# Performance work log

Measured on AMD Instinct MI355X. Metric: run time of the kernel, lower is better.

## Reference

```python
import jax, jax.numpy as jnp
import numpy as np

N, E = 50000, 800000
NODE_IN, EDGE_IN = 32, 16
EMB, GEMB = 128, 128
H, C, L, B = 4, 32, 2, 8   # heads, per-head dim, layers, graphs
GAT_IN = NODE_IN + EMB      # skip_conn=True
NEG_SLOPE = 0.2
EPS = 1e-5


def layernorm(x, g, b):
    m = jnp.mean(x, -1, keepdims=True)
    v = jnp.mean((x - m) ** 2, -1, keepdims=True)
    return (x - m) / jnp.sqrt(v + EPS) * g + b


def setup_inputs() -> dict:
    key = jax.random.key(0)
    ks = jax.random.split(key, 24)
    s = 0.05
    return {
        "x": jax.random.normal(ks[0], (N, NODE_IN), jnp.float32),
        "edge_attr": jax.random.normal(ks[1], (E, EDGE_IN), jnp.float32),
        "W_in": jax.random.normal(ks[2], (NODE_IN, EMB), jnp.float32) * s,
        "b_in": jnp.zeros((EMB,), jnp.float32),
        "W_src": jax.random.normal(ks[3], (L, GAT_IN, H * C), jnp.float32) * s,
        "W_edge": jax.random.normal(ks[4], (L, EDGE_IN, H * C), jnp.float32) * s,
        "att_src": jax.random.normal(ks[5], (L, H, C), jnp.float32) * s,
        "att_dst": jax.random.normal(ks[6], (L, H, C), jnp.float32) * s,
        "att_edge": jax.random.normal(ks[7], (L, H, C), jnp.float32) * s,
        "gat_bias": jnp.zeros((L, H * C), jnp.float32),
        "ln_gamma": jnp.ones((L, EMB), jnp.float32),
        "ln_beta": jnp.zeros((L, EMB), jnp.float32),
        "W_out": jax.random.normal(ks[8], (EMB, EMB), jnp.float32) * s,
        "b_out": jnp.zeros((EMB,), jnp.float32),
        "ln_out_gamma": jnp.ones((EMB,), jnp.float32),
        "ln_out_beta": jnp.zeros((EMB,), jnp.float32),
        "W_g": jax.random.normal(ks[9], (EMB, GEMB), jnp.float32) * s,
        "b_g": jnp.zeros((GEMB,), jnp.float32),
        "g_gamma": jnp.ones((GEMB,), jnp.float32),
        "g_beta": jnp.zeros((GEMB,), jnp.float32),
        "edge_index": jax.random.randint(ks[10], (2, E), 0, N, jnp.int32),
        "batch": jnp.sort(jax.random.randint(ks[11], (N,), 0, B, jnp.int32)),
    }


def reference(x, edge_attr, W_in, b_in, W_src, W_edge, att_src, att_dst, att_edge,
              gat_bias, ln_gamma, ln_beta, W_out, b_out, ln_out_gamma, ln_out_beta,
              W_g, b_g, g_gamma, g_beta, edge_index, batch):
    # PyG GATConv adds self-loops with edge_attr fill_value='mean'
    loop = jnp.arange(N, dtype=edge_index.dtype)
    src = jnp.concatenate([edge_index[0], loop])   # [E2]
    dst = jnp.concatenate([edge_index[1], loop])   # [E2]
    ea = jnp.concatenate([edge_attr, jnp.broadcast_to(edge_attr.mean(0), (N, EDGE_IN))], 0)

    h = jax.nn.relu(x @ W_in + b_in)  # [N, EMB]
    for l in range(L):
        inp = jnp.concatenate([x, h], -1)                   # skip connection [N, GAT_IN]
        xs = (inp @ W_src[l]).reshape(N, H, C)              # projected nodes
        a_s = jnp.einsum('nhc,hc->nh', xs, att_src[l])
        a_d = jnp.einsum('nhc,hc->nh', xs, att_dst[l])
        ee = (ea @ W_edge[l]).reshape(-1, H, C)             # [E2, H, C]
        a_e = jnp.einsum('ehc,hc->eh', ee, att_edge[l])
        alpha = jax.nn.leaky_relu(a_s[src] + a_d[dst] + a_e, NEG_SLOPE)  # [E2, H]
        # segment softmax over incoming edges of each destination node
        amax = jax.ops.segment_max(alpha, dst, num_segments=N)
        ex = jnp.exp(alpha - amax[dst])
        denom = jax.ops.segment_sum(ex, dst, num_segments=N)
        w = ex / (denom[dst] + 1e-16)
        msg = xs[src] * w[:, :, None]                        # [E2, H, C]
        out = jax.ops.segment_sum(msg, dst, num_segments=N).reshape(N, H * C) + gat_bias[l]
        h = jax.nn.elu(layernorm(out, ln_gamma[l], ln_beta[l]))

    g = layernorm(jax.nn.relu(h @ W_g + b_g), g_gamma, g_beta)
    gsum = jax.ops.segment_sum(g, batch, num_segments=B)
    cnt = jax.ops.segment_sum(jnp.ones((N, 1), g.dtype), batch, num_segments=B)
    graph_embeddings = gsum / jnp.maximum(cnt, 1.0)

    node_embeddings = layernorm(jax.nn.relu(h @ W_out + b_out), ln_out_gamma, ln_out_beta)
    return node_embeddings, graph_embeddings
```

## Files before the change

kernel.cpp:

```cpp
#include <hip/hip_runtime.h>

#define N_NODES 50000
#define N_EDGES 800000
#define E2      850000
#define NODE_IN 32
#define EDGE_IN 16
#define EMB     128
#define GAT_IN  160
#define NLAYER  2
#define NGRAPH  8
#define NBLK    196
#define NB32    1563
#define NB64    782

#define GWT_SRC0 0
#define GWT_SRC1 20480
#define GWT_OUT  40960
#define GWT_G    57344
#define GWT_TOT  73728

typedef short bf16x8 __attribute__((ext_vector_type(8)));
typedef float f32x4 __attribute__((ext_vector_type(4)));

__device__ __forceinline__ unsigned int f2bf(float f) {
    unsigned int u = __float_as_uint(f);
    return (u + 0x7FFFu + ((u >> 16) & 1u)) >> 16;
}
__device__ __forceinline__ float bf2f(unsigned int h) {
    return __uint_as_float(h << 16);
}
__device__ __forceinline__ unsigned int pack2bf(float a, float b) {
    return f2bf(a) | (f2bf(b) << 16);
}

__global__ void zero_kernel(float* __restrict__ p, int n) {
    int i = blockIdx.x * blockDim.x + threadIdx.x;
    int stride = gridDim.x * blockDim.x;
    for (; i < n; i += stride) p[i] = 0.f;
}

__global__ __launch_bounds__(256) void mean_kernel(const float* __restrict__ ea,
                                                   float* __restrict__ meta) {
    __shared__ float sm[16];
    int t = threadIdx.x;
    if (t < 16) sm[t] = 0.f;
    __syncthreads();
    int gid = blockIdx.x * 256 + t;
    int q = gid & 3;
    const float4* ea4 = (const float4*)ea;
    float4 s = make_float4(0.f, 0.f, 0.f, 0.f);
    for (int j = gid; j < N_EDGES * 4; j += 2048 * 256) {
        float4 v = ea4[j];
        s.x += v.x; s.y += v.y; s.z += v.z; s.w += v.w;
    }
    atomicAdd(&sm[q * 4 + 0], s.x);
    atomicAdd(&sm[q * 4 + 1], s.y);
    atomicAdd(&sm[q * 4 + 2], s.z);
    atomicAdd(&sm[q * 4 + 3], s.w);
    __syncthreads();
    if (t < 16) atomicAdd(&meta[t], sm[t]);
}

__global__ void prep_kernel(const float* __restrict__ W_edge,
                            const float* __restrict__ att_edge,
                            float* __restrict__ meta) {
    int t = threadIdx.x;
    if (t < EDGE_IN) meta[t] = meta[t] * (1.0f / (float)N_EDGES);
    __syncthreads();
    {
        int l = t >> 6, k = (t >> 2) & 15, h = t & 3;
        const float* w = W_edge + ((size_t)l * EDGE_IN + k) * EMB + h * 32;
        const float* a = att_edge + (size_t)l * EMB + h * 32;
        float acc = 0.f;
#pragma unroll
        for (int c = 0; c < 32; c++) acc += w[c] * a[c];
        meta[16 + (l * 16 + k) * 4 + h] = acc;
    }
    __syncthreads();
    if (t < 8) {
        int l = t >> 2, h = t & 3;
        float acc = 0.f;
#pragma unroll
        for (int k = 0; k < EDGE_IN; k++) acc += meta[k] * meta[16 + (l * 16 + k) * 4 + h];
        meta[144 + t] = acc;
    }
}

__global__ __launch_bounds__(256) void prep_wt_kernel(const float* __restrict__ Wsrc,
                                                      const float* __restrict__ Wout,
                                                      const float* __restrict__ Wg,
                                                      unsigned short* __restrict__ gwt) {
    int g = blockIdx.x * 256 + threadIdx.x;
    const float* Wm;
    int base, gg;
    if (g < 5120) {
        int l = g / 2560;
        gg = g - l * 2560;
        Wm = Wsrc + (size_t)l * GAT_IN * EMB;
        base = l * 20480;
    } else if (g < 7168) {
        gg = g - 5120;
        Wm = Wout;
        base = GWT_OUT;
    } else {
        gg = g - 7168;
        Wm = Wg;
        base = GWT_G;
    }
    int lane = gg & 63, tmp = gg >> 6;
    int nt = tmp & 7, kc = tmp >> 3;
    int quad = lane >> 4, l16 = lane & 15;
    int col = nt * 16 + l16, k0 = kc * 32 + quad * 8;
    unsigned int u[4];
#pragma unroll
    for (int j = 0; j < 4; j++)
        u[j] = pack2bf(Wm[(size_t)(k0 + 2 * j) * EMB + col], Wm[(size_t)(k0 + 2 * j + 1) * EMB + col]);
    *(uint4*)(gwt + base + (size_t)gg * 8) = make_uint4(u[0], u[1], u[2], u[3]);
}

__global__ __launch_bounds__(256) void count_rank_kernel(const int* __restrict__ edge_index,
                                                         int* __restrict__ cnt4,
                                                         int* __restrict__ rank) {
    int e = blockIdx.x * 256 + threadIdx.x;
    if (e >= E2) return;
    int dst = (e < N_EDGES) ? edge_index[N_EDGES + e] : (e - N_EDGES);
    int shard = blockIdx.x & 3;
    rank[e] = atomicAdd(&cnt4[shard * N_NODES + dst], 1);
}

__global__ __launch_bounds__(256) void scan1_kernel(const int* __restrict__ cnt4,
                                                    int* __restrict__ bsum) {
    __shared__ int sm[256];
    int t = threadIdx.x;
    int i = blockIdx.x * 256 + t;
    int tot = 0;
    if (i < N_NODES) {
#pragma unroll
        for (int s = 0; s < 4; s++) tot += cnt4[s * N_NODES + i];
    }
    sm[t] = tot;
    __syncthreads();
#pragma unroll
    for (int d = 128; d >= 1; d >>= 1) {
        if (t < d) sm[t] += sm[t + d];
        __syncthreads();
    }
    if (t == 0) bsum[blockIdx.x] = sm[0];
}

__global__ __launch_bounds__(256) void scan2_kernel(const int* __restrict__ bsum,
                                                    int* __restrict__ bbase) {
    __shared__ int sm[256];
    int t = threadIdx.x;
    int v = (t < NBLK) ? bsum[t] : 0;
    sm[t] = v;
    __syncthreads();
#pragma unroll
    for (int d = 1; d < 256; d <<= 1) {
        int u = (t >= d) ? sm[t - d] : 0;
        __syncthreads();
        sm[t] += u;
        __syncthreads();
    }
    if (t < NBLK) bbase[t] = sm[t] - v;
}

__global__ __launch_bounds__(256) void scan3_kernel(const int* __restrict__ bbase,
                                                    const int* __restrict__ cnt4,
                                                    int* __restrict__ off,
                                                    int* __restrict__ shard_base) {
    __shared__ int sm[256];
    int t = threadIdx.x;
    int i = blockIdx.x * 256 + t;
    int c[4] = {0, 0, 0, 0};
    int tot = 0;
    if (i < N_NODES) {
#pragma unroll
        for (int s = 0; s < 4; s++) {
            c[s] = cnt4[s * N_NODES + i];
            tot += c[s];
        }
    }
    sm[t] = tot;
    __syncthreads();
#pragma unroll
    for (int d = 1; d < 256; d <<= 1) {
        int u = (t >= d) ? sm[t - d] : 0;
        __syncthreads();
        sm[t] += u;
        __syncthreads();
    }
    if (i < N_NODES) {
        int base = bbase[blockIdx.x] + sm[t] - tot;
        off[i] = base;
        int4 sb;
        sb.x = base;            base += c[0];
        sb.y = base;            base += c[1];
        sb.z = base;            base += c[2];
        sb.w = base;
        *(int4*)(shard_base + i * 4) = sb;
        if (i == N_NODES - 1) off[N_NODES] = E2;
    }
}

__global__ __launch_bounds__(256) void fill_ae_kernel(const int* __restrict__ edge_index,
                                                      const float* __restrict__ edge_attr,
                                                      const float* __restrict__ meta,
                                                      const int* __restrict__ rank,
                                                      const int* __restrict__ shard_base,
                                                      int* __restrict__ csr_src,
                                                      float* __restrict__ csr_ae0,
                                                      float* __restrict__ csr_ae1) {
    __shared__ float Ml[128];
    __shared__ float loop_ae[8];
    int t = threadIdx.x;
    if (t < 128) Ml[t] = meta[16 + t];
    if (t < 8) loop_ae[t] = meta[144 + t];
    __syncthreads();
    int e = blockIdx.x * 256 + t;
    if (e >= E2) return;
    int src, dst;
    float ae[2][4];
    if (e < N_EDGES) {
        src = edge_index[e];
        dst = edge_index[N_EDGES + e];
        const float4* r4 = (const float4*)(edge_attr + (size_t)e * EDGE_IN);
#pragma unroll
        for (int l = 0; l < 2; l++)
#pragma unroll
            for (int h = 0; h < 4; h++) ae[l][h] = 0.f;
#pragma unroll
        for (int q = 0; q < 4; q++) {
            float4 v = r4[q];
#pragma unroll
            for (int l = 0; l < 2; l++) {
                const float* M = Ml + l * 64;
#pragma unroll
                for (int h = 0; h < 4; h++) {
                    ae[l][h] += v.x * M[(4 * q + 0) * 4 + h] + v.y * M[(4 * q + 1) * 4 + h] +
                                v.z * M[(4 * q + 2) * 4 + h] + v.w * M[(4 * q + 3) * 4 + h];
                }
            }
        }
    } else {
        src = dst = e - N_EDGES;
#pragma unroll
        for (int l = 0; l < 2; l++)
#pragma unroll
            for (int h = 0; h < 4; h++) ae[l][h] = loop_ae[l * 4 + h];
    }
    int shard = (e >> 8) & 3;
    int pos = shard_base[dst * 4 + shard] + rank[e];
    csr_src[pos] = src;
    *(float4*)(csr_ae0 + (size_t)pos * 4) = make_float4(ae[0][0], ae[0][1], ae[0][2], ae[0][3]);
    *(float4*)(csr_ae1 + (size_t)pos * 4) = make_float4(ae[1][0], ae[1][1], ae[1][2], ae[1][3]);
}

__global__ __launch_bounds__(256) void input_proj_kernel(const float* __restrict__ x,
                                                         const float* __restrict__ W,
                                                         const float* __restrict__ b,
                                                         unsigned int* __restrict__ h_bf,
                                                         unsigned int* __restrict__ x_bf) {
    __shared__ float inp[32][NODE_IN];
    int t = threadIdx.x;
    int n0 = blockIdx.x * 32;
    for (int i = t; i < 32 * NODE_IN; i += 256) {
        int r = i >> 5, c = i & 31;
        int n = min(n0 + r, N_NODES - 1);
        inp[r][c] = x[(size_t)n * NODE_IN + c];
    }
    __syncthreads();
    for (int i = t; i < 32 * 16; i += 256) {
        int r = i >> 4, c = i & 15;
        int n = n0 + r;
        if (n < N_NODES) x_bf[(size_t)n * 16 + c] = pack2bf(inp[r][2 * c], inp[r][2 * c + 1]);
    }
    int wave = t >> 6, lane = t & 63;
    int c0 = lane * 2, c1 = c0 + 1;
    const float2* W2 = (const float2*)W;
    float acc[8][2];
#pragma unroll
    for (int j = 0; j < 8; j++) { acc[j][0] = b[c0]; acc[j][1] = b[c1]; }
#pragma unroll 2
    for (int k4 = 0; k4 < NODE_IN / 4; k4++) {
        float4 v[8];
#pragma unroll
        for (int j = 0; j < 8; j++) v[j] = *(const float4*)&inp[wave * 8 + j][k4 * 4];
#pragma unroll
        for (int kk = 0; kk < 4; kk++) {
            float2 w = W2[(k4 * 4 + kk) * 64 + lane];
#pragma unroll
            for (int j = 0; j < 8; j++) {
                float vv = (&v[j].x)[kk];
                acc[j][0] += vv * w.x;
                acc[j][1] += vv * w.y;
            }
        }
    }
#pragma unroll
    for (int j = 0; j < 8; j++) {
        int n = n0 + wave * 8 + j;
        if (n < N_NODES)
            h_bf[(size_t)n * 64 + lane] = pack2bf(fmaxf(acc[j][0], 0.f), fmaxf(acc[j][1], 0.f));
    }
}

template <int K, int MODE>
__global__ __launch_bounds__(256) void dense_mfma_kernel(
    const unsigned int* __restrict__ xbf, const unsigned int* __restrict__ hbf,
    const unsigned short* __restrict__ gwt, const float* __restrict__ bias,
    const float* __restrict__ v1, const float* __restrict__ v2,
    const int* __restrict__ batch,
    unsigned int* __restrict__ xs_out, float* __restrict__ a_s, float* __restrict__ a_d,
    float* __restrict__ out_nodes, float* __restrict__ gsum, float* __restrict__ gcnt) {
    constexpr int CLS = 132;
    __shared__ __align__(16) float cl[64 * CLS];
    __shared__ float red[(MODE != 0) ? 64 : 1][8];
    __shared__ float locw[(MODE == 2) ? 4 : 1][2][EMB];
    __shared__ int bids[(MODE == 2) ? 64 : 1];

    int t = threadIdx.x;
    int n0 = blockIdx.x * 64;
    if (MODE == 2 && t < 64) bids[t] = batch[min(n0 + t, N_NODES - 1)];

    int wave = t >> 6, lane = t & 63;
    int quad = lane >> 4, l16 = lane & 15;
    int arow = min(n0 + wave * 16 + l16, N_NODES - 1);
    const bf16x8* B = (const bf16x8*)gwt;
    f32x4 acc[8];
#pragma unroll
    for (int i = 0; i < 8; i++) acc[i] = (f32x4){0.f, 0.f, 0.f, 0.f};
#pragma unroll
    for (int kc = 0; kc < K / 32; kc++) {
        bf16x8 af;
        if (MODE == 0 && kc == 0) {
            af = *(const bf16x8*)(xbf + (size_t)arow * 16 + quad * 4);
        } else {
            int hk = ((MODE == 0) ? (kc - 1) : kc) * 16;
            af = *(const bf16x8*)(hbf + (size_t)arow * 64 + hk + quad * 4);
        }
#pragma unroll
        for (int nt = 0; nt < 8; nt++) {
            bf16x8 bfv = B[(kc * 8 + nt) * 64 + lane];
            acc[nt] = __builtin_amdgcn_mfma_f32_16x16x32_bf16(af, bfv, acc[nt], 0, 0, 0);
        }
    }
#pragma unroll
    for (int nt = 0; nt < 8; nt++) {
#pragma unroll
        for (int i = 0; i < 4; i++) {
            int r = wave * 16 + quad * 4 + i;
            cl[r * CLS + nt * 16 + l16] = acc[nt][i];
        }
    }
    __syncthreads();

    int p = t & 3, r = t >> 2;
    int n = n0 + r;
    const float4* c4 = (const float4*)(cl + r * CLS + p * 32);

    if (MODE == 0) {
        const float4* s4 = (const float4*)(v1 + p * 32);
        const float4* d4 = (const float4*)(v2 + p * 32);
        if (n < N_NODES) {
            float s_ = 0.f, d_ = 0.f;
#pragma unroll
            for (int i = 0; i < 8; i++) {
                float4 cv = c4[i], sv = s4[i], dv = d4[i];
                s_ += cv.x * sv.x + cv.y * sv.y + cv.z * sv.z + cv.w * sv.w;
                d_ += cv.x * dv.x + cv.y * dv.y + cv.z * dv.z + cv.w * dv.w;
                uint2 pk = make_uint2(pack2bf(cv.x, cv.y), pack2bf(cv.z, cv.w));
                *(uint2*)(xs_out + (size_t)n * 64 + p * 16 + 2 * i) = pk;
            }
            a_s[(size_t)n * 4 + p] = s_;
            a_d[(size_t)n * 4 + p] = d_;
        }
    } else {
        const float4* b4 = (const float4*)(bias + p * 32);
        float vals[32];
        float s_ = 0.f, q_ = 0.f;
#pragma unroll
        for (int i = 0; i < 8; i++) {
            float4 cv = c4[i], bv = b4[i];
            float w0 = fmaxf(cv.x + bv.x, 0.f), w1 = fmaxf(cv.y + bv.y, 0.f);
            float w2 = fmaxf(cv.z + bv.z, 0.f), w3 = fmaxf(cv.w + bv.w, 0.f);
            vals[4 * i] = w0; vals[4 * i + 1] = w1; vals[4 * i + 2] = w2; vals[4 * i + 3] = w3;
            s_ += w0 + w1 + w2 + w3;
            q_ += w0 * w0 + w1 * w1 + w2 * w2 + w3 * w3;
        }
        red[r][p] = s_;
        red[r][4 + p] = q_;
        __syncthreads();
        float sm = red[r][0] + red[r][1] + red[r][2] + red[r][3];
        float sq = red[r][4] + red[r][5] + red[r][6] + red[r][7];
        float mean = sm * (1.f / EMB);
        float var = sq * (1.f / EMB) - mean * mean;
        float rstd = rsqrtf(var + 1e-5f);
        const float4* g4 = (const float4*)(v1 + p * 32);
        const float4* be4 = (const float4*)(v2 + p * 32);
#pragma unroll
        for (int i = 0; i < 8; i++) {
            float4 gv = g4[i], bv = be4[i];
            vals[4 * i]     = (vals[4 * i]     - mean) * rstd * gv.x + bv.x;
            vals[4 * i + 1] = (vals[4 * i + 1] - mean) * rstd * gv.y + bv.y;
            vals[4 * i + 2] = (vals[4 * i + 2] - mean) * rstd * gv.z + bv.z;
            vals[4 * i + 3] = (vals[4 * i + 3] - mean) * rstd * gv.w + bv.w;
        }
        if (MODE == 1) {
            if (n < N_NODES) {
                float* op = out_nodes + (size_t)n * EMB + p * 32;
#pragma unroll
                for (int i = 0; i < 8; i++)
                    *(float4*)(op + 4 * i) = make_float4(vals[4 * i], vals[4 * i + 1],
                                                         vals[4 * i + 2], vals[4 * i + 3]);
            }
        } else {
            int nvalid = min(64, N_NODES - n0);
            int bmin = bids[0], bmax = bids[nvalid - 1];
            int bid = bids[r];
            bool inA = (bid == bmin) && (n < N_NODES);
            bool inB = (bid == bmax) && (bmax != bmin) && (n < N_NODES);
            if (n < N_NODES && bid != bmin && bid != bmax) {
#pragma unroll
                for (int i = 0; i < 32; i++)
                    atomicAdd(&gsum[(size_t)bid * EMB + p * 32 + i], vals[i]);
            }
#pragma unroll
            for (int g = 0; g < 2; g++) {
                bool m = g ? inB : inA;
#pragma unroll
                for (int i = 0; i < 32; i++) {
                    float v = m ? vals[i] : 0.f;
                    v += __shfl_xor(v, 4, 64);
                    v += __shfl_xor(v, 8, 64);
                    v += __shfl_xor(v, 16, 64);
                    v += __shfl_xor(v, 32, 64);
                    if ((lane >> 2) == 0) locw[wave][g][(lane & 3) * 32 + i] = v;
                }
            }
            __syncthreads();
            if (t < 128) {
                float sA = locw[0][0][t] + locw[1][0][t] + locw[2][0][t] + locw[3][0][t];
                atomicAdd(&gsum[(size_t)bmin * EMB + t], sA);
                if (bmax != bmin) {
                    float sB = locw[0][1][t] + locw[1][1][t] + locw[2][1][t] + locw[3][1][t];
                    atomicAdd(&gsum[(size_t)bmax * EMB + t], sB);
                }
            } else if (t == 255) {
                int cA = 0, cB = 0;
                for (int rr = 0; rr < nvalid; rr++) {
                    int bb = bids[rr];
                    if (bb == bmin) cA++;
                    else if (bb == bmax) cB++;
                    else atomicAdd(&gcnt[bb], 1.f);
                }
                atomicAdd(&gcnt[bmin], (float)cA);
                if (bmax != bmin && cB > 0) atomicAdd(&gcnt[bmax], (float)cB);
            }
        }
    }
}

__global__ __launch_bounds__(256) void gat_gather_kernel(const int* __restrict__ off,
                                                         const int* __restrict__ csr_src,
                                                         const float* __restrict__ csr_ae,
                                                         const unsigned int* __restrict__ xs,
                                                         const float* __restrict__ a_s,
                                                         const float* __restrict__ a_d,
                                                         const float* __restrict__ bias_l,
                                                         const float* __restrict__ gamma_l,
                                                         const float* __restrict__ beta_l,
                                                         unsigned int* __restrict__ h_bf) {
    int t = threadIdx.x, wave = t >> 6, lane = t & 63;
    int n = blockIdx.x * 4 + wave;
    int c0 = lane * 2, c1 = c0 + 1;
    int h = lane >> 4;
    float ad = a_d[(size_t)n * 4 + h];
    int p0 = __builtin_amdgcn_readfirstlane(off[n]);
    int p1 = __builtin_amdgcn_readfirstlane(off[n + 1]);
    float den = 0.f, acc0 = 0.f, acc1 = 0.f;
    int p = p0;
    for (; p + 1 < p1; p += 2) {
        int sA = csr_src[p], sB = csr_src[p + 1];
        float aeA = csr_ae[(size_t)p * 4 + h];
        float aeB = csr_ae[(size_t)(p + 1) * 4 + h];
        float asA = a_s[(size_t)sA * 4 + h];
        float asB = a_s[(size_t)sB * 4 + h];
        unsigned int vA = xs[(size_t)sA * 64 + lane];
        unsigned int vB = xs[(size_t)sB * 64 + lane];
        float alA = asA + ad + aeA;
        alA = alA > 0.f ? alA : 0.2f * alA;
        float exA = __expf(alA);
        float alB = asB + ad + aeB;
        alB = alB > 0.f ? alB : 0.2f * alB;
        float exB = __expf(alB);
        den += exA + exB;
        acc0 += exA * bf2f(vA & 0xFFFFu) + exB * bf2f(vB & 0xFFFFu);
        acc1 += exA * bf2f(vA >> 16) + exB * bf2f(vB >> 16);
    }
    if (p < p1) {
        int s = csr_src[p];
        float ae = csr_ae[(size_t)p * 4 + h];
        float as = a_s[(size_t)s * 4 + h];
        unsigned int v = xs[(size_t)s * 64 + lane];
        float al = as + ad + ae;
        al = al > 0.f ? al : 0.2f * al;
        float ex = __expf(al);
        den += ex;
        acc0 += ex * bf2f(v & 0xFFFFu);
        acc1 += ex * bf2f(v >> 16);
    }
    float dinv = 1.0f / (den + 1e-16f);
    float v0 = acc0 * dinv + bias_l[c0];
    float v1 = acc1 * dinv + bias_l[c1];
    float sm = v0 + v1, sq = v0 * v0 + v1 * v1;
#pragma unroll
    for (int o = 32; o >= 1; o >>= 1) {
        sm += __shfl_down(sm, o, 64);
        sq += __shfl_down(sq, o, 64);
    }
    sm = __shfl(sm, 0, 64);
    sq = __shfl(sq, 0, 64);
    float mean = sm * (1.f / EMB);
    float var = sq * (1.f / EMB) - mean * mean;
    float rstd = rsqrtf(var + 1e-5f);
    float y0 = (v0 - mean) * rstd * gamma_l[c0] + beta_l[c0];
    float y1 = (v1 - mean) * rstd * gamma_l[c1] + beta_l[c1];
    y0 = y0 > 0.f ? y0 : __expf(y0) - 1.f;
    y1 = y1 > 0.f ? y1 : __expf(y1) - 1.f;
    h_bf[(size_t)n * 64 + lane] = pack2bf(y0, y1);
}

__global__ void graph_out_kernel(const float* __restrict__ gsum, const float* __restrict__ gcnt,
                                 float* __restrict__ out) {
    int i = blockIdx.x * blockDim.x + threadIdx.x;
    if (i >= NGRAPH * EMB) return;
    int b = i >> 7;
    float c = fmaxf(gcnt[b], 1.f);
    out[(size_t)N_NODES * EMB + i] = gsum[i] / c;
}

extern "C" void kernel_launch(void* const* d_in, const int* in_sizes, int n_in,
                              void* d_out, int out_size, void* d_ws, size_t ws_size,
                              hipStream_t stream) {
    (void)in_sizes; (void)n_in; (void)out_size; (void)ws_size;
    const float* x         = (const float*)d_in[0];
    const float* edge_attr = (const float*)d_in[1];
    const float* W_in      = (const float*)d_in[2];
    const float* b_in      = (const float*)d_in[3];
    const float* W_src     = (const float*)d_in[4];
    const float* W_edge    = (const float*)d_in[5];
    const float* att_src   = (const float*)d_in[6];
    const float* att_dst   = (const float*)d_in[7];
    const float* att_edge  = (const float*)d_in[8];
    const float* gat_bias  = (const float*)d_in[9];
    const float* ln_gamma  = (const float*)d_in[10];
    const float* ln_beta   = (const float*)d_in[11];
    const float* W_out     = (const float*)d_in[12];
    const float* b_out     = (const float*)d_in[13];
    const float* ln_og     = (const float*)d_in[14];
    const float* ln_ob     = (const float*)d_in[15];
    const float* W_g       = (const float*)d_in[16];
    const float* b_g       = (const float*)d_in[17];
    const float* g_gamma   = (const float*)d_in[18];
    const float* g_beta    = (const float*)d_in[19];
    const int* edge_index  = (const int*)d_in[20];
    const int* batch       = (const int*)d_in[21];
    float* out = (float*)d_out;

    float* ws              = (float*)d_ws;
    unsigned int* h_bf     = (unsigned int*)ws;
    unsigned int* xs       = h_bf + (size_t)N_NODES * 64;
    unsigned int* x_bf     = xs + (size_t)N_NODES * 64;
    float* a_s             = (float*)(x_bf + (size_t)N_NODES * 16);
    float* a_d             = a_s + (size_t)N_NODES * 4;
    float* csr_ae          = a_d + (size_t)N_NODES * 4;
    unsigned short* gwt    = (unsigned short*)(csr_ae + (size_t)2 * E2 * 4);
    float* meta            = (float*)(gwt + GWT_TOT);
    float* gsum            = meta + 152;
    float* gcnt            = gsum + NGRAPH * EMB;
    int*   cnt4            = (int*)(gcnt + NGRAPH);
    int*   off             = cnt4 + 4 * N_NODES;
    int*   shard_base      = off + N_NODES + 1;
    int*   rank            = shard_base + 4 * N_NODES;
    int*   csr_src         = rank + E2;
    int*   bsum            = csr_src + E2;
    int*   bbase           = bsum + NBLK;

    const int EB = (E2 + 255) / 256;

    zero_kernel<<<256, 256, 0, stream>>>(meta, 152 + NGRAPH * EMB + NGRAPH + 4 * N_NODES);
    mean_kernel<<<2048, 256, 0, stream>>>(edge_attr, meta);
    prep_kernel<<<1, 128, 0, stream>>>(W_edge, att_edge, meta);
    prep_wt_kernel<<<36, 256, 0, stream>>>(W_src, W_out, W_g, gwt);
    input_proj_kernel<<<NB32, 256, 0, stream>>>(x, W_in, b_in, h_bf, x_bf);

    count_rank_kernel<<<EB, 256, 0, stream>>>(edge_index, cnt4, rank);
    scan1_kernel<<<NBLK, 256, 0, stream>>>(cnt4, bsum);
    scan2_kernel<<<1, 256, 0, stream>>>(bsum, bbase);
    scan3_kernel<<<NBLK, 256, 0, stream>>>(bbase, cnt4, off, shard_base);
    fill_ae_kernel<<<EB, 256, 0, stream>>>(edge_index, edge_attr, meta, rank, shard_base,
                                           csr_src, csr_ae, csr_ae + (size_t)E2 * 4);

    for (int l = 0; l < NLAYER; l++) {
        dense_mfma_kernel<GAT_IN, 0><<<NB64, 256, 0, stream>>>(
            x_bf, h_bf, gwt + (l ? GWT_SRC1 : GWT_SRC0), nullptr,
            att_src + (size_t)l * EMB, att_dst + (size_t)l * EMB, nullptr,
            xs, a_s, a_d, nullptr, nullptr, nullptr);
        gat_gather_kernel<<<N_NODES / 4, 256, 0, stream>>>(
            off, csr_src, csr_ae + (size_t)l * E2 * 4, xs, a_s, a_d,
            gat_bias + (size_t)l * EMB, ln_gamma + (size_t)l * EMB,
            ln_beta + (size_t)l * EMB, h_bf);
    }

    dense_mfma_kernel<EMB, 1><<<NB64, 256, 0, stream>>>(
        nullptr, h_bf, gwt + GWT_OUT, b_out, ln_og, ln_ob, nullptr,
        nullptr, nullptr, nullptr, out, nullptr, nullptr);
    dense_mfma_kernel<EMB, 2><<<NB64, 256, 0, stream>>>(
        nullptr, h_bf, gwt + GWT_G, b_g, g_gamma, g_beta, batch,
        nullptr, nullptr, nullptr, nullptr, gsum, gcnt);
    graph_out_kernel<<<4, 256, 0, stream>>>(gsum, gcnt, out);
}
```

Baseline: 470.0 us.

## Fuse count with mean, split CSR fill via permutation, widen gather loads

Merges edge counting and the edge-attribute mean into one kernel to save a launch. CSR construction is split: a small kernel scatters (src, edge id) pairs into a permutation buffer, and a second kernel reads edge_attr by edge id and writes the attention terms contiguously, replacing wide scattered float4 stores with one int2 scatter. The gather kernel now handles 8 edges per iteration, with four lane groups each loading 16-byte feature chunks; it reduces across groups with shuffles and only group 0 writes. This aims for more memory-level parallelism and fewer, wider loads, at the cost of an extra kernel pass and gathered reads of edge_attr.

```diff
diff --git a/kernel.cpp b/kernel.cpp
--- a/kernel.cpp
+++ b/kernel.cpp
@@ -39,26 +39,37 @@
     for (; i < n; i += stride) p[i] = 0.f;
 }
 
-__global__ __launch_bounds__(256) void mean_kernel(const float* __restrict__ ea,
-                                                   float* __restrict__ meta) {
+__global__ __launch_bounds__(256) void count_mean_kernel(const int* __restrict__ edge_index,
+                                                         const float* __restrict__ edge_attr,
+                                                         int* __restrict__ cnt4,
+                                                         int* __restrict__ rank,
+                                                         float* __restrict__ meta) {
     __shared__ float sm[16];
     int t = threadIdx.x;
-    if (t < 16) sm[t] = 0.f;
-    __syncthreads();
-    int gid = blockIdx.x * 256 + t;
-    int q = gid & 3;
-    const float4* ea4 = (const float4*)ea;
-    float4 s = make_float4(0.f, 0.f, 0.f, 0.f);
-    for (int j = gid; j < N_EDGES * 4; j += 2048 * 256) {
-        float4 v = ea4[j];
-        s.x += v.x; s.y += v.y; s.z += v.z; s.w += v.w;
-    }
-    atomicAdd(&sm[q * 4 + 0], s.x);
-    atomicAdd(&sm[q * 4 + 1], s.y);
-    atomicAdd(&sm[q * 4 + 2], s.z);
-    atomicAdd(&sm[q * 4 + 3], s.w);
-    __syncthreads();
-    if (t < 16) atomicAdd(&meta[t], sm[t]);
+    int e = blockIdx.x * 256 + t;
+    if (e < E2) {
+        int dst = (e < N_EDGES) ? edge_index[N_EDGES + e] : (e - N_EDGES);
+        int shard = blockIdx.x & 3;
+        rank[e] = atomicAdd(&cnt4[shard * N_NODES + dst], 1);
+    }
+    if (blockIdx.x < 512) {
+        if (t < 16) sm[t] = 0.f;
+        __syncthreads();
+        int gid = blockIdx.x * 256 + t;
+        int q = gid & 3;
+        const float4* ea4 = (const float4*)edge_attr;
+        float4 s = make_float4(0.f, 0.f, 0.f, 0.f);
+        for (int j = gid; j < N_EDGES * 4; j += 512 * 256) {
+            float4 v = ea4[j];
+            s.x += v.x; s.y += v.y; s.z += v.z; s.w += v.w;
+        }
+        atomicAdd(&sm[q * 4 + 0], s.x);
+        atomicAdd(&sm[q * 4 + 1], s.y);
+        atomicAdd(&sm[q * 4 + 2], s.z);
+        atomicAdd(&sm[q * 4 + 3], s.w);
+        __syncthreads();
+        if (t < 16) atomicAdd(&meta[t], sm[t]);
+    }
 }
 
 __global__ void prep_kernel(const float* __restrict__ W_edge,
@@ -118,16 +129,6 @@
     *(uint4*)(gwt + base + (size_t)gg * 8) = make_uint4(u[0], u[1], u[2], u[3]);
 }
 
-__global__ __launch_bounds__(256) void count_rank_kernel(const int* __restrict__ edge_index,
-                                                         int* __restrict__ cnt4,
-                                                         int* __restrict__ rank) {
-    int e = blockIdx.x * 256 + threadIdx.x;
-    if (e >= E2) return;
-    int dst = (e < N_EDGES) ? edge_index[N_EDGES + e] : (e - N_EDGES);
-    int shard = blockIdx.x & 3;
-    rank[e] = atomicAdd(&cnt4[shard * N_NODES + dst], 1);
-}
-
 __global__ __launch_bounds__(256) void scan1_kernel(const int* __restrict__ cnt4,
                                                     int* __restrict__ bsum) {
     __shared__ int sm[256];
@@ -203,32 +204,48 @@
     }
 }
 
-__global__ __launch_bounds__(256) void fill_ae_kernel(const int* __restrict__ edge_index,
-                                                      const float* __restrict__ edge_attr,
-                                                      const float* __restrict__ meta,
-                                                      const int* __restrict__ rank,
-                                                      const int* __restrict__ shard_base,
-                                                      int* __restrict__ csr_src,
-                                                      float* __restrict__ csr_ae0,
-                                                      float* __restrict__ csr_ae1) {
-    __shared__ float Ml[128];
-    __shared__ float loop_ae[8];
-    int t = threadIdx.x;
-    if (t < 128) Ml[t] = meta[16 + t];
-    if (t < 8) loop_ae[t] = meta[144 + t];
-    __syncthreads();
-    int e = blockIdx.x * 256 + t;
+__global__ __launch_bounds__(256) void fill_perm_kernel(const int* __restrict__ edge_index,
+                                                        const int* __restrict__ rank,
+                                                        const int* __restrict__ shard_base,
+                                                        int* __restrict__ perm) {
+    int e = blockIdx.x * 256 + threadIdx.x;
     if (e >= E2) return;
     int src, dst;
-    float ae[2][4];
     if (e < N_EDGES) {
         src = edge_index[e];
         dst = edge_index[N_EDGES + e];
+    } else {
+        src = dst = e - N_EDGES;
+    }
+    int shard = (e >> 8) & 3;
+    int pos = shard_base[dst * 4 + shard] + rank[e];
+    ((int2*)perm)[pos] = make_int2(src, e);
+}
+
+__global__ __launch_bounds__(256) void compute_ae_kernel(const int* __restrict__ perm,
+                                                         const float* __restrict__ edge_attr,
+                                                         const float* __restrict__ meta,
+                                                         int* __restrict__ csr_src,
+                                                         float* __restrict__ csr_ae0,
+                                                         float* __restrict__ csr_ae1) {
+    __shared__ float Ml[128];
+    __shared__ float loop_ae[8];
+    int t = threadIdx.x;
+    if (t < 128) Ml[t] = meta[16 + t];
+    if (t < 8) loop_ae[t] = meta[144 + t];
+    __syncthreads();
+    int p = blockIdx.x * 256 + t;
+    if (p >= E2) return;
+    int2 pe = ((const int2*)perm)[p];
+    int src = pe.x, e = pe.y;
+    csr_src[p] = src;
+    float ae[2][4];
+    if (e < N_EDGES) {
         const float4* r4 = (const float4*)(edge_attr + (size_t)e * EDGE_IN);
 #pragma unroll
         for (int l = 0; l < 2; l++)
 #pragma unroll
-            for (int h = 0; h < 4; h++) ae[l][h] = 0.f;
+            for (int hh = 0; hh < 4; hh++) ae[l][hh] = 0.f;
 #pragma unroll
         for (int q = 0; q < 4; q++) {
             float4 v = r4[q];
@@ -236,24 +253,20 @@
             for (int l = 0; l < 2; l++) {
                 const float* M = Ml + l * 64;
 #pragma unroll
-                for (int h = 0; h < 4; h++) {
-                    ae[l][h] += v.x * M[(4 * q + 0) * 4 + h] + v.y * M[(4 * q + 1) * 4 + h] +
-                                v.z * M[(4 * q + 2) * 4 + h] + v.w * M[(4 * q + 3) * 4 + h];
+                for (int hh = 0; hh < 4; hh++) {
+                    ae[l][hh] += v.x * M[(4 * q + 0) * 4 + hh] + v.y * M[(4 * q + 1) * 4 + hh] +
+                                 v.z * M[(4 * q + 2) * 4 + hh] + v.w * M[(4 * q + 3) * 4 + hh];
                 }
             }
         }
     } else {
-        src = dst = e - N_EDGES;
 #pragma unroll
         for (int l = 0; l < 2; l++)
 #pragma unroll
-            for (int h = 0; h < 4; h++) ae[l][h] = loop_ae[l * 4 + h];
-    }
-    int shard = (e >> 8) & 3;
-    int pos = shard_base[dst * 4 + shard] + rank[e];
-    csr_src[pos] = src;
-    *(float4*)(csr_ae0 + (size_t)pos * 4) = make_float4(ae[0][0], ae[0][1], ae[0][2], ae[0][3]);
-    *(float4*)(csr_ae1 + (size_t)pos * 4) = make_float4(ae[1][0], ae[1][1], ae[1][2], ae[1][3]);
+            for (int hh = 0; hh < 4; hh++) ae[l][hh] = loop_ae[l * 4 + hh];
+    }
+    *(float4*)(csr_ae0 + (size_t)p * 4) = make_float4(ae[0][0], ae[0][1], ae[0][2], ae[0][3]);
+    *(float4*)(csr_ae1 + (size_t)p * 4) = make_float4(ae[1][0], ae[1][1], ae[1][2], ae[1][3]);
 }
 
 __global__ __launch_bounds__(256) void input_proj_kernel(const float* __restrict__ x,
@@ -473,62 +486,94 @@
                                                          unsigned int* __restrict__ h_bf) {
     int t = threadIdx.x, wave = t >> 6, lane = t & 63;
     int n = blockIdx.x * 4 + wave;
-    int c0 = lane * 2, c1 = c0 + 1;
-    int h = lane >> 4;
+    int g = lane >> 4, l16 = lane & 15;
+    int h = l16 >> 2;
     float ad = a_d[(size_t)n * 4 + h];
     int p0 = __builtin_amdgcn_readfirstlane(off[n]);
     int p1 = __builtin_amdgcn_readfirstlane(off[n + 1]);
-    float den = 0.f, acc0 = 0.f, acc1 = 0.f;
-    int p = p0;
-    for (; p + 1 < p1; p += 2) {
-        int sA = csr_src[p], sB = csr_src[p + 1];
-        float aeA = csr_ae[(size_t)p * 4 + h];
-        float aeB = csr_ae[(size_t)(p + 1) * 4 + h];
+    int plast = p1 - 1;
+    float den = 0.f;
+    float acc[8];
+#pragma unroll
+    for (int j = 0; j < 8; j++) acc[j] = 0.f;
+
+    for (int pb = p0; pb < p1; pb += 8) {
+        int pA = pb + g, pB = pb + 4 + g;
+        int iA = min(pA, plast), iB = min(pB, plast);
+        int sA = csr_src[iA], sB = csr_src[iB];
+        float aeA = csr_ae[(size_t)iA * 4 + h];
+        float aeB = csr_ae[(size_t)iB * 4 + h];
         float asA = a_s[(size_t)sA * 4 + h];
         float asB = a_s[(size_t)sB * 4 + h];
-        unsigned int vA = xs[(size_t)sA * 64 + lane];
-        unsigned int vB = xs[(size_t)sB * 64 + lane];
+        uint4 xA = *(const uint4*)(xs + (size_t)sA * 64 + l16 * 4);
+        uint4 xB = *(const uint4*)(xs + (size_t)sB * 64 + l16 * 4);
         float alA = asA + ad + aeA;
         alA = alA > 0.f ? alA : 0.2f * alA;
-        float exA = __expf(alA);
+        float exA = (pA <= plast) ? __expf(alA) : 0.f;
         float alB = asB + ad + aeB;
         alB = alB > 0.f ? alB : 0.2f * alB;
-        float exB = __expf(alB);
+        float exB = (pB <= plast) ? __expf(alB) : 0.f;
         den += exA + exB;
-        acc0 += exA * bf2f(vA & 0xFFFFu) + exB * bf2f(vB & 0xFFFFu);
-        acc1 += exA * bf2f(vA >> 16) + exB * bf2f(vB >> 16);
-    }
-    if (p < p1) {
-        int s = csr_src[p];
-        float ae = csr_ae[(size_t)p * 4 + h];
-        float as = a_s[(size_t)s * 4 + h];
-        unsigned int v = xs[(size_t)s * 64 + lane];
-        float al = as + ad + ae;
-        al = al > 0.f ? al : 0.2f * al;
-        float ex = __expf(al);
-        den += ex;
-        acc0 += ex * bf2f(v & 0xFFFFu);
-        acc1 += ex * bf2f(v >> 16);
-    }
+        unsigned int u;
+        u = xA.x; acc[0] += exA * bf2f(u & 0xFFFFu); acc[1] += exA * bf2f(u >> 16);
+        u = xA.y; acc[2] += exA * bf2f(u & 0xFFFFu); acc[3] += exA * bf2f(u >> 16);
+        u = xA.z; acc[4] += exA * bf2f(u & 0xFFFFu); acc[5] += exA * bf2f(u >> 16);
+        u = xA.w; acc[6] += exA * bf2f(u & 0xFFFFu); acc[7] += exA * bf2f(u >> 16);
+        u = xB.x; acc[0] += exB * bf2f(u & 0xFFFFu); acc[1] += exB * bf2f(u >> 16);
+        u = xB.y; acc[2] += exB * bf2f(u & 0xFFFFu); acc[3] += exB * bf2f(u >> 16);
+        u = xB.z; acc[4] += exB * bf2f(u & 0xFFFFu); acc[5] += exB * bf2f(u >> 16);
+        u = xB.w; acc[6] += exB * bf2f(u & 0xFFFFu); acc[7] += exB * bf2f(u >> 16);
+    }
+#pragma unroll
+    for (int j = 0; j < 8; j++) {
+        acc[j] += __shfl_xor(acc[j], 16, 64);
+        acc[j] += __shfl_xor(acc[j], 32, 64);
+    }
+    den += __shfl_xor(den, 16, 64);
+    den += __shfl_xor(den, 32, 64);
+
     float dinv = 1.0f / (den + 1e-16f);
-    float v0 = acc0 * dinv + bias_l[c0];
-    float v1 = acc1 * dinv + bias_l[c1];
-    float sm = v0 + v1, sq = v0 * v0 + v1 * v1;
-#pragma unroll
-    for (int o = 32; o >= 1; o >>= 1) {
-        sm += __shfl_down(sm, o, 64);
-        sq += __shfl_down(sq, o, 64);
-    }
-    sm = __shfl(sm, 0, 64);
-    sq = __shfl(sq, 0, 64);
+    int c0 = l16 * 8;
+    const float4* b4 = (const float4*)(bias_l + c0);
+    float4 bv0 = b4[0], bv1 = b4[1];
+    float v[8];
+    v[0] = acc[0] * dinv + bv0.x; v[1] = acc[1] * dinv + bv0.y;
+    v[2] = acc[2] * dinv + bv0.z; v[3] = acc[3] * dinv + bv0.w;
+    v[4] = acc[4] * dinv + bv1.x; v[5] = acc[5] * dinv + bv1.y;
+    v[6] = acc[6] * dinv + bv1.z; v[7] = acc[7] * dinv + bv1.w;
+    float sm = 0.f, sq = 0.f;
+#pragma unroll
+    for (int j = 0; j < 8; j++) { sm += v[j]; sq += v[j] * v[j]; }
+#pragma unroll
+    for (int o = 1; o <= 8; o <<= 1) {
+        sm += __shfl_xor(sm, o, 64);
+        sq += __shfl_xor(sq, o, 64);
+    }
     float mean = sm * (1.f / EMB);
     float var = sq * (1.f / EMB) - mean * mean;
     float rstd = rsqrtf(var + 1e-5f);
-    float y0 = (v0 - mean) * rstd * gamma_l[c0] + beta_l[c0];
-    float y1 = (v1 - mean) * rstd * gamma_l[c1] + beta_l[c1];
-    y0 = y0 > 0.f ? y0 : __expf(y0) - 1.f;
-    y1 = y1 > 0.f ? y1 : __expf(y1) - 1.f;
-    h_bf[(size_t)n * 64 + lane] = pack2bf(y0, y1);
+    const float4* g4 = (const float4*)(gamma_l + c0);
+    const float4* be4 = (const float4*)(beta_l + c0);
+    float4 gv0 = g4[0], gv1 = g4[1], bev0 = be4[0], bev1 = be4[1];
+    float y[8];
+    y[0] = (v[0] - mean) * rstd * gv0.x + bev0.x;
+    y[1] = (v[1] - mean) * rstd * gv0.y + bev0.y;
+    y[2] = (v[2] - mean) * rstd * gv0.z + bev0.z;
+    y[3] = (v[3] - mean) * rstd * gv0.w + bev0.w;
+    y[4] = (v[4] - mean) * rstd * gv1.x + bev1.x;
+    y[5] = (v[5] - mean) * rstd * gv1.y + bev1.y;
+    y[6] = (v[6] - mean) * rstd * gv1.z + bev1.z;
+    y[7] = (v[7] - mean) * rstd * gv1.w + bev1.w;
+#pragma unroll
+    for (int j = 0; j < 8; j++) y[j] = y[j] > 0.f ? y[j] : __expf(y[j]) - 1.f;
+    if (g == 0) {
+        uint4 o4;
+        o4.x = pack2bf(y[0], y[1]);
+        o4.y = pack2bf(y[2], y[3]);
+        o4.z = pack2bf(y[4], y[5]);
+        o4.w = pack2bf(y[6], y[7]);
+        *(uint4*)(h_bf + (size_t)n * 64 + l16 * 4) = o4;
+    }
 }
 
 __global__ void graph_out_kernel(const float* __restrict__ gsum, const float* __restrict__ gcnt,
@@ -586,21 +631,22 @@
     int*   csr_src         = rank + E2;
     int*   bsum            = csr_src + E2;
     int*   bbase           = bsum + NBLK;
+    int*   perm            = (int*)xs;
 
     const int EB = (E2 + 255) / 256;
 
     zero_kernel<<<256, 256, 0, stream>>>(meta, 152 + NGRAPH * EMB + NGRAPH + 4 * N_NODES);
-    mean_kernel<<<2048, 256, 0, stream>>>(edge_attr, meta);
+    count_mean_kernel<<<EB, 256, 0, stream>>>(edge_index, edge_attr, cnt4, rank, meta);
     prep_kernel<<<1, 128, 0, stream>>>(W_edge, att_edge, meta);
     prep_wt_kernel<<<36, 256, 0, stream>>>(W_src, W_out, W_g, gwt);
     input_proj_kernel<<<NB32, 256, 0, stream>>>(x, W_in, b_in, h_bf, x_bf);
 
-    count_rank_kernel<<<EB, 256, 0, stream>>>(edge_index, cnt4, rank);
     scan1_kernel<<<NBLK, 256, 0, stream>>>(cnt4, bsum);
     scan2_kernel<<<1, 256, 0, stream>>>(bsum, bbase);
     scan3_kernel<<<NBLK, 256, 0, stream>>>(bbase, cnt4, off, shard_base);
-    fill_ae_kernel<<<EB, 256, 0, stream>>>(edge_index, edge_attr, meta, rank, shard_base,
-                                           csr_src, csr_ae, csr_ae + (size_t)E2 * 4);
+    fill_perm_kernel<<<EB, 256, 0, stream>>>(edge_index, rank, shard_base, perm);
+    compute_ae_kernel<<<EB, 256, 0, stream>>>(perm, edge_attr, meta,
+                                              csr_src, csr_ae, csr_ae + (size_t)E2 * 4);
 
     for (int l = 0; l < NLAYER; l++) {
         dense_mfma_kernel<GAT_IN, 0><<<NB64, 256, 0, stream>>>(
```

Result: faster. 432.6 us (-8.0%).
